# Performance work log

Hardware: AMD Instinct MI355X
Metric: run time of the kernel (lower is better)

## Reference

```python
import jax, jax.numpy as jnp
import numpy as np

N = 20000; P = 3; L_LP = 10; L_NS = 20; D = 128; OUT = 2; E = 640000; V_LP = 5000; V_NS = 10000


def _gru(x, lengths, W_ih, W_hh, b_ih, b_hh):
    # x: [B, T, Din]; returns last valid hidden state per sequence (pack_padded semantics)
    T = x.shape[1]
    xp = jnp.einsum('btd,gd->btg', x, W_ih) + b_ih  # [B, T, 3H]
    h0 = jnp.zeros((x.shape[0], W_hh.shape[1]), x.dtype)

    def step(h, inp):
        xpt, t = inp
        hp = h @ W_hh.T + b_hh
        xr, xz, xn = jnp.split(xpt, 3, axis=-1)
        hr, hz, hn = jnp.split(hp, 3, axis=-1)
        r = jax.nn.sigmoid(xr + hr)
        z = jax.nn.sigmoid(xz + hz)
        nn_ = jnp.tanh(xn + r * hn)
        h_new = (1.0 - z) * nn_ + z * h
        h = jnp.where((t < lengths)[:, None], h_new, h)
        return h, None

    hT, _ = jax.lax.scan(step, h0, (jnp.swapaxes(xp, 0, 1), jnp.arange(T)))
    return hT


def _gcn(x, src, dst, w, W, b, n):
    # PyG GCNConv: add self-loops (weight 1), symmetric normalization by in-degree
    loops = jnp.arange(n)
    s = jnp.concatenate([src, loops])
    d = jnp.concatenate([dst, loops])
    ww = jnp.concatenate([w, jnp.ones((n,), w.dtype)])
    deg = jax.ops.segment_sum(ww, d, num_segments=n)
    dinv = jnp.where(deg > 0, 1.0 / jnp.sqrt(deg), 0.0)
    norm = dinv[s] * ww * dinv[d]
    xw = x @ W.T
    return jax.ops.segment_sum(norm[:, None] * xw[s], d, num_segments=n) + b


def _lnorm(x, g, b):
    m = jnp.mean(x, axis=-1, keepdims=True)
    v = jnp.var(x, axis=-1, keepdims=True)
    return (x - m) / jnp.sqrt(v + 1e-5) * g + b


def _forward(x_ref, x_def, x_pdt, edge_weight, lp_emb, ns_emb, lp_Wih, lp_Whh, lp_bih, lp_bhh, ns_Wih, ns_Whh, ns_bih, ns_bhh, lp_fc_W, lp_fc_b, all_fc_W, all_fc_b, conv1_W, conv1_b, conv2_W, conv2_b, conv3_W, conv3_b, ln1_g, ln1_b, ln2_g, ln2_b, mp1_W, mp1_b, mp2_W, mp2_b, idx_lp, x_lp_length, idx_ns, x_ns_length, edge_index):
    n = idx_ns.shape[0]
    # long-path GRU encodings, one GRU run per path slot (vmapped over P)
    xl = lp_emb[idx_lp]  # [N, P, L_LP, D]
    gru_lp = lambda seq, lens: _gru(seq, lens, lp_Wih, lp_Whh, lp_bih, lp_bhh)
    h_lp = jax.vmap(gru_lp, in_axes=(1, 1))(xl, x_lp_length)  # [P, N, D]
    # torch.cat(h_list).view(N, D*P): row-major reshape of [P, N, D]
    x_lp = h_lp.reshape(n, P * D) @ lp_fc_W.T + lp_fc_b
    # natural-sequence GRU encoding
    x_ns = _gru(ns_emb[idx_ns], x_ns_length, ns_Wih, ns_Whh, ns_bih, ns_bhh)  # [N, D]
    # torch.cat(dim=0).view(N, 5D): faithful row-major reshape of [5N, D]
    x = jnp.concatenate([x_pdt, x_ref, x_def, x_lp, x_ns], axis=0).reshape(n, 5 * D)
    x = x @ all_fc_W.T + all_fc_b
    src, dst = edge_index[0], edge_index[1]
    convs = [(conv1_W, conv1_b), (conv2_W, conv2_b), (conv3_W, conv3_b)]
    lns = [(ln1_g, ln1_b), (ln2_g, ln2_b)]
    emb = x
    for i in range(3):
        x = _gcn(x, src, dst, edge_weight, convs[i][0], convs[i][1], n)
        emb = x
        x = jax.nn.relu(x)
        # dropout p=0.25 omitted (eval mode)
        if i < 2:
            x = _lnorm(x, lns[i][0], lns[i][1])
    x = x @ mp1_W.T + mp1_b
    x = x @ mp2_W.T + mp2_b
    return emb, jax.nn.log_softmax(x, axis=1)


def setup_inputs() -> dict:
    ks = jax.random.split(jax.random.key(0), 40)
    f32 = jnp.float32
    nrm = lambda k, sh, s: jax.random.normal(k, sh, f32) * s
    inp = {}
    inp['idx_lp'] = jax.random.randint(ks[0], (N, P, L_LP), 0, V_LP)
    inp['x_lp_length'] = jax.random.randint(ks[1], (N, P), 1, L_LP + 1)
    inp['idx_ns'] = jax.random.randint(ks[2], (N, L_NS), 0, V_NS)
    inp['x_ns_length'] = jax.random.randint(ks[3], (N,), 1, L_NS + 1)
    inp['x_ref'] = nrm(ks[4], (N, D), 1.0)
    inp['x_def'] = nrm(ks[5], (N, D), 1.0)
    inp['x_pdt'] = nrm(ks[6], (N, D), 1.0)
    inp['edge_index'] = jax.random.randint(ks[7], (2, E), 0, N)
    inp['edge_weight'] = jax.random.uniform(ks[8], (E,), f32)
    inp['lp_emb'] = nrm(ks[9], (V_LP, D), 0.5)
    inp['ns_emb'] = nrm(ks[10], (V_NS, D), 0.5)
    s = 0.08
    inp['lp_Wih'] = nrm(ks[11], (3 * D, D), s)
    inp['lp_Whh'] = nrm(ks[12], (3 * D, D), s)
    inp['lp_bih'] = nrm(ks[13], (3 * D,), s)
    inp['lp_bhh'] = nrm(ks[14], (3 * D,), s)
    inp['ns_Wih'] = nrm(ks[15], (3 * D, D), s)
    inp['ns_Whh'] = nrm(ks[16], (3 * D, D), s)
    inp['ns_bih'] = nrm(ks[17], (3 * D,), s)
    inp['ns_bhh'] = nrm(ks[18], (3 * D,), s)
    inp['lp_fc_W'] = nrm(ks[19], (D, P * D), 0.05)
    inp['lp_fc_b'] = nrm(ks[20], (D,), 0.05)
    inp['all_fc_W'] = nrm(ks[21], (D, 5 * D), 0.05)
    inp['all_fc_b'] = nrm(ks[22], (D,), 0.05)
    inp['conv1_W'] = nrm(ks[23], (D, D), 0.08)
    inp['conv1_b'] = nrm(ks[24], (D,), 0.05)
    inp['conv2_W'] = nrm(ks[25], (D, D), 0.08)
    inp['conv2_b'] = nrm(ks[26], (D,), 0.05)
    inp['conv3_W'] = nrm(ks[27], (D, D), 0.08)
    inp['conv3_b'] = nrm(ks[28], (D,), 0.05)
    inp['ln1_g'] = jnp.ones((D,), f32)
    inp['ln1_b'] = jnp.zeros((D,), f32)
    inp['ln2_g'] = jnp.ones((D,), f32)
    inp['ln2_b'] = jnp.zeros((D,), f32)
    inp['mp1_W'] = nrm(ks[29], (D, D), 0.08)
    inp['mp1_b'] = nrm(ks[30], (D,), 0.05)
    inp['mp2_W'] = nrm(ks[31], (OUT, D), 0.08)
    inp['mp2_b'] = nrm(ks[32], (OUT,), 0.05)
    return inp


def reference(idx_lp, x_lp_length, idx_ns, x_ns_length, x_ref, x_def, x_pdt, edge_index, edge_weight, lp_emb, ns_emb, lp_Wih, lp_Whh, lp_bih, lp_bhh, ns_Wih, ns_Whh, ns_bih, ns_bhh, lp_fc_W, lp_fc_b, all_fc_W, all_fc_b, conv1_W, conv1_b, conv2_W, conv2_b, conv3_W, conv3_b, ln1_g, ln1_b, ln2_g, ln2_b, mp1_W, mp1_b, mp2_W, mp2_b):
    return _forward(x_ref, x_def, x_pdt, edge_weight, lp_emb, ns_emb, lp_Wih, lp_Whh, lp_bih, lp_bhh, ns_Wih, ns_Whh, ns_bih, ns_bhh, lp_fc_W, lp_fc_b, all_fc_W, all_fc_b, conv1_W, conv1_b, conv2_W, conv2_b, conv3_W, conv3_b, ln1_g, ln1_b, ln2_g, ln2_b, mp1_W, mp1_b, mp2_W, mp2_b, idx_lp, x_lp_length, idx_ns, x_ns_length, edge_index)
```

## Files before the change

kernel.cpp:

```cpp
#include <hip/hip_runtime.h>
#include <math.h>

typedef unsigned short u16;
typedef short bf16x4 __attribute__((ext_vector_type(4)));
typedef short bf16x8 __attribute__((ext_vector_type(8)));
typedef float f32x16 __attribute__((ext_vector_type(16)));

#define NN 20000
#define PP 3
#define TLP 10
#define TNS 20
#define DD 128
#define EE 640000

__device__ __forceinline__ float bf2f(u16 u) {
  union { unsigned u; float f; } v; v.u = ((unsigned)u) << 16; return v.f;
}
__device__ __forceinline__ u16 f2bf(float f) {
  union { float f; unsigned u; } v; v.f = f;
  unsigned r = v.u + 0x7fffu + ((v.u >> 16) & 1u);
  return (u16)(r >> 16);
}
__device__ __forceinline__ short f2bf_hw(float f) {
  __bf16 b = (__bf16)f;
  return (short)__builtin_bit_cast(unsigned short, b);
}
__device__ __forceinline__ float loadf(const void* p, size_t i, int isf) {
  return isf ? ((const float*)p)[i] : bf2f(((const u16*)p)[i]);
}
__device__ __forceinline__ float fex2(float x) { return __builtin_amdgcn_exp2f(x); }
__device__ __forceinline__ float frcp(float x) { return __builtin_amdgcn_rcpf(x); }
__device__ __forceinline__ unsigned cvtpk(float lo, float hi) {
  unsigned r; asm("v_cvt_pk_bf16_f32 %0, %1, %2" : "=v"(r) : "v"(lo), "v"(hi));
  return r;
}

__global__ void k_detect(const void* probe, int* flag, int* bins) {
  __shared__ int any;
  if (threadIdx.x == 0) any = 0;
  __syncthreads();
  if (threadIdx.x < 128) bins[threadIdx.x] = 0;
  const u16* p = (const u16*)probe;
  int bad = 0;
  for (int i = threadIdx.x; i < 4096; i += 256) {
    int e = (p[2 * i] >> 7) & 0xFF;
    if (e >= 0x9F) bad = 1;
  }
  if (bad) atomicOr(&any, 1);
  __syncthreads();
  if (threadIdx.x == 0) flag[0] = any;
}

struct CvtJobs {
  const void* src[16];
  int off[16];
  int n[16];
};

struct CvtJobsB {
  const void* src[12];
  int off[12];
  int n[12];
  int thr[12];
  float scA[12];
  float scB[12];
};

__global__ void k_cvtb(CvtJobsB j, CvtJobs jf, u16* __restrict__ dst,
                       float* __restrict__ fdst, int* __restrict__ counts,
                       const int* flag) {
  const int isf = flag[0];
  if (blockIdx.x >= 12 * 64 + 16) {
    int i = (blockIdx.x - (12 * 64 + 16)) * 256 + threadIdx.x;
    if (i < NN) counts[i] = 0;
    return;
  }
  if (blockIdx.x >= 12 * 64) {
    const int job = blockIdx.x - 12 * 64;
    const void* s = jf.src[job];
    float* d = fdst + jf.off[job];
    const int n = jf.n[job];
    for (int i = threadIdx.x; i < n; i += 256) d[i] = loadf(s, i, isf);
    return;
  }
  const int job = blockIdx.x >> 6;
  if (job < 2 && !isf) return;
  const int chunk = blockIdx.x & 63;
  const void* s = j.src[job];
  u16* d = dst + j.off[job];
  const int n = j.n[job];
  const int thr = j.thr[job];
  const float sA = j.scA[job], sB = j.scB[job];
  for (int i = chunk * 256 + threadIdx.x; i < n; i += 64 * 256)
    d[i] = f2bf(loadf(s, i, isf) * (i < thr ? sA : sB));
}

__global__ void k_lenboth(const int* __restrict__ lensLP,
                          const int* __restrict__ lensNS,
                          int* __restrict__ bins,
                          const int* __restrict__ e_dst,
                          int* __restrict__ counts) {
  const int nLen = (PP * NN + 255) / 256;
  if ((int)blockIdx.x >= nLen) {
    int e = ((int)blockIdx.x - nLen) * 256 + threadIdx.x;
    if (e < EE) atomicAdd(&counts[e_dst[e]], 1);
    return;
  }
  int sg = blockIdx.x * 256 + threadIdx.x;
  int lane = threadIdx.x & 63;
  int binL = 0, binN = 0;
  if (sg < PP * NN) binL = lensLP[(sg % NN) * PP + sg / NN];
  if (sg < NN) binN = lensNS[sg];
  for (int b = 1; b <= TLP; ++b) {
    unsigned long long m = __ballot(binL == b);
    if (m) {
      int leader = (int)(__ffsll((long long)m) - 1);
      if (lane == leader) atomicAdd(&bins[b], (int)__popcll(m));
    }
  }
  for (int b = 1; b <= TNS; ++b) {
    unsigned long long m = __ballot(binN == b);
    if (m) {
      int leader = (int)(__ffsll((long long)m) - 1);
      if (lane == leader) atomicAdd(&bins[64 + b], (int)__popcll(m));
    }
  }
}

__global__ void k_binscan2(int* __restrict__ bins,
                           const float* __restrict__ w_mp2,
                           const float* __restrict__ b_mp1_,
                           const float* __restrict__ b_mp2_,
                           const void* __restrict__ mp1raw,
                           float* __restrict__ Wc, const int* flag) {
  if (blockIdx.x == 0) {
    if (threadIdx.x == 0) {
      int acc = 0;
      for (int k = 0; k < 32; ++k) { bins[32 + k] = acc; acc += bins[k]; }
    }
    if (threadIdx.x == 1) {
      int acc = 0;
      for (int k = 0; k < 32; ++k) { bins[96 + k] = acc; acc += bins[64 + k]; }
    }
    return;
  }
  const int isf = flag[0];
  const int t = threadIdx.x;
  const int o = t >> 7, k = t & 127;
  float acc = 0.f;
  for (int d2 = 0; d2 < 128; ++d2)
    acc += w_mp2[o * 128 + d2] * loadf(mp1raw, (size_t)d2 * 128 + k, isf);
  Wc[t] = acc;
  if (t < 2) {
    float bacc = b_mp2_[t];
    for (int d2 = 0; d2 < 128; ++d2) bacc += w_mp2[t * 128 + d2] * b_mp1_[d2];
    Wc[256 + t] = bacc;
  }
}

__global__ void k_lenfillboth(const int* __restrict__ lensLP,
                              const int* __restrict__ lensNS,
                              int* __restrict__ bins,
                              int* __restrict__ permLP,
                              int* __restrict__ permNS) {
  int sg = blockIdx.x * 256 + threadIdx.x;
  int lane = threadIdx.x & 63;
  int binL = 0, binN = 0;
  if (sg < PP * NN) binL = lensLP[(sg % NN) * PP + sg / NN];
  if (sg < NN) binN = lensNS[sg];
  for (int b = 1; b <= TLP; ++b) {
    unsigned long long m = __ballot(binL == b);
    if (m) {
      int leader = (int)(__ffsll((long long)m) - 1);
      int base = 0;
      if (lane == leader) base = atomicAdd(&bins[32 + b], (int)__popcll(m));
      base = __shfl(base, leader);
      if (binL == b) {
        int rank = (int)__popcll(m & ((1ull << lane) - 1ull));
        permLP[base + rank] = sg;
      }
    }
  }
  for (int b = 1; b <= TNS; ++b) {
    unsigned long long m = __ballot(binN == b);
    if (m) {
      int leader = (int)(__ffsll((long long)m) - 1);
      int base = 0;
      if (lane == leader) base = atomicAdd(&bins[96 + b], (int)__popcll(m));
      base = __shfl(base, leader);
      if (binN == b) {
        int rank = (int)__popcll(m & ((1ull << lane) - 1ull));
        permNS[base + rank] = sg;
      }
    }
  }
}

__global__ __launch_bounds__(512, 2) void k_gru5(
    const int* __restrict__ permLP, const int* __restrict__ permNS, int nbNS,
    const u16* __restrict__ embLPc, const u16* __restrict__ embNSc,
    const u16* __restrict__ embLPr, const u16* __restrict__ embNSr,
    const int* __restrict__ idxLP, const int* __restrict__ idxNS,
    const int* __restrict__ lenLP, const int* __restrict__ lenNS,
    const u16* __restrict__ WihLP, const u16* __restrict__ WhhLP,
    const u16* __restrict__ WihNS, const u16* __restrict__ WhhNS,
    const float* __restrict__ bihLP, const float* __restrict__ bhhLP,
    const float* __restrict__ bihNS, const float* __restrict__ bhhNS,
    u16* __restrict__ HoutLP, u16* __restrict__ HoutNS, int nbLP,
    const int* __restrict__ counts, int* __restrict__ startA,
    int* __restrict__ cursorE, const int* __restrict__ flag) {
  __shared__ u16 xp[2][3][128][36];
  __shared__ u16 Hbf2[2][32][132];
  __shared__ int ivs[TNS][32];
  __shared__ int rowv[32], outv[32], lenv_s[32];
  __shared__ int Tbs;

  const int tid = threadIdx.x;
  if (blockIdx.x == 0) {
    int* part = (int*)ivs;
    const int C = (NN + 255) / 256;
    if (tid < 256) {
      int base = tid * C;
      int s = 0;
      for (int k = 0; k < C; ++k) {
        int i2 = base + k;
        s += (i2 < NN) ? counts[i2] : 0;
      }
      part[tid] = s;
    }
    __syncthreads();
    if (tid == 0) {
      int acc = 0;
      for (int k = 0; k < 256; ++k) { int v = part[k]; part[k] = acc; acc += v; }
    }
    __syncthreads();
    if (tid < 256) {
      int run = part[tid];
      int base = tid * C;
      for (int k = 0; k < C; ++k) {
        int i2 = base + k;
        if (i2 < NN) {
          int c = counts[i2];
          startA[i2] = run;
          cursorE[i2] = run;
          run += c;
        }
      }
      if (tid == 255) startA[NN] = run;
    }
    return;
  }
  const int bid = blockIdx.x - 1;
  const int isf = flag[0];
  const int isNS = bid < nbNS;
  const int chunk = isNS ? (nbNS - 1 - bid) : (nbLP - 1 - (bid - nbNS));
  const int* perm = isNS ? (permNS + chunk * 32) : (permLP + chunk * 32);
  const u16* embbf = isNS ? (isf ? embNSc : embNSr) : (isf ? embLPc : embLPr);
  const int* idx = isNS ? idxNS : idxLP;
  const int* lens = isNS ? lenNS : lenLP;
  const u16* Wih = isNS ? WihNS : WihLP;
  const u16* Whh = isNS ? WhhNS : WhhLP;
  const float* bih = isNS ? bihNS : bihLP;
  const float* bhh = isNS ? bhhNS : bhhLP;
  u16* Hout = isNS ? HoutNS : HoutLP;
  const int T = isNS ? TNS : TLP;

  const int w = tid >> 6, lane = tid & 63;
  const int l31 = lane & 31, lh = lane >> 5;
  const int role = w >> 2;
  const int j = w & 3;
  const int d = 32 * j + l31;

  if (tid < 32) {
    int sg = perm[tid];
    int row = isNS ? sg : ((sg % NN) * PP + sg / NN);
    rowv[tid] = row;
    outv[tid] = sg;
    lenv_s[tid] = lens[row];
  }
  __syncthreads();
  if (tid == 0) {
    int m = 1;
    for (int k = 0; k < 32; ++k) m = max(m, lenv_s[k]);
    Tbs = m;
  }
  __syncthreads();
  const int Tb = Tbs;

  for (int z = tid; z < Tb * 32; z += 512) {
    int s = z & 31, t = z >> 5;
    ivs[t][s] = idx[(size_t)rowv[s] * T + t];
  }
  for (int z = tid; z < 2112; z += 512) ((unsigned*)Hbf2[0])[z] = 0u;

  bf16x8 wf[24];
  {
    const u16* Ws = role ? Whh : Wih;
#pragma unroll
    for (int g = 0; g < 3; ++g)
#pragma unroll
      for (int kb = 0; kb < 8; ++kb)
        wf[g * 8 + kb] =
            *(const bf16x8*)(Ws + (size_t)(128 * g + d) * 128 + kb * 16 + lh * 8);
  }
  const float SA = -1.44269504088896f;
  const float SN = -2.88539008177793f;
  float ib0, ib1, ib2;
  if (!role) {
    ib0 = SA * (bih[d] + bhh[d]);
    ib1 = SA * (bih[128 + d] + bhh[128 + d]);
    ib2 = SN * bih[256 + d];
  } else {
    ib0 = 0.f;
    ib1 = 0.f;
    ib2 = SN * bhh[256 + d];
  }

  __syncthreads();
  int lenr[16];
#pragma unroll
  for (int rg = 0; rg < 16; ++rg)
    lenr[rg] = lenv_s[(rg & 3) + 8 * (rg >> 2) + 4 * lh];

  float h[16];
#pragma unroll
  for (int rg = 0; rg < 16; ++rg) h[rg] = 0.f;

  for (int i = 0; i <= Tb; ++i) {
    if (!role) {
      if (i < Tb) {
        bf16x8 Xf[8];
        const u16* erow = embbf + (size_t)ivs[i][l31] * 128 + lh * 8;
#pragma unroll
        for (int kb = 0; kb < 8; ++kb) Xf[kb] = *(const bf16x8*)(erow + kb * 16);
        f32x16 a0 = (f32x16)(ib0), a1 = (f32x16)(ib1), a2 = (f32x16)(ib2);
#pragma unroll
        for (int kb = 0; kb < 8; ++kb) {
          a0 = __builtin_amdgcn_mfma_f32_32x32x16_bf16(Xf[kb], wf[kb], a0, 0, 0, 0);
          a1 = __builtin_amdgcn_mfma_f32_32x32x16_bf16(Xf[kb], wf[8 + kb], a1, 0, 0, 0);
          a2 = __builtin_amdgcn_mfma_f32_32x32x16_bf16(Xf[kb], wf[16 + kb], a2, 0, 0, 0);
        }
        const int sl = i & 1;
#pragma unroll
        for (int rq = 0; rq < 4; ++rq) {
          int mo = 8 * rq + 4 * lh;
          bf16x4 p0, p1, p2;
#pragma unroll
          for (int q = 0; q < 4; ++q) {
            p0[q] = f2bf_hw(a0[4 * rq + q]);
            p1[q] = f2bf_hw(a1[4 * rq + q]);
            p2[q] = f2bf_hw(a2[4 * rq + q]);
          }
          *(bf16x4*)(&xp[sl][0][d][mo]) = p0;
          *(bf16x4*)(&xp[sl][1][d][mo]) = p1;
          *(bf16x4*)(&xp[sl][2][d][mo]) = p2;
        }
      }
    } else {
      if (i >= 1) {
        const int rs = (i - 1) & 1, wsl = i & 1;
        bf16x8 Hf[8];
#pragma unroll
        for (int kb = 0; kb < 8; ++kb) {
          bf16x4 lo = *(const bf16x4*)(&Hbf2[rs][l31][16 * kb + 8 * lh]);
          bf16x4 hi = *(const bf16x4*)(&Hbf2[rs][l31][16 * kb + 8 * lh + 4]);
          Hf[kb] = __builtin_shufflevector(lo, hi, 0, 1, 2, 3, 4, 5, 6, 7);
        }
        f32x16 a0 = (f32x16)(ib0), a1 = (f32x16)(ib1), a2 = (f32x16)(ib2);
#pragma unroll
        for (int kb = 0; kb < 8; ++kb) {
          a0 = __builtin_amdgcn_mfma_f32_32x32x16_bf16(Hf[kb], wf[kb], a0, 0, 0, 0);
          a1 = __builtin_amdgcn_mfma_f32_32x32x16_bf16(Hf[kb], wf[8 + kb], a1, 0, 0, 0);
          a2 = __builtin_amdgcn_mfma_f32_32x32x16_bf16(Hf[kb], wf[16 + kb], a2, 0, 0, 0);
        }
        const int t = i - 1;
#pragma unroll
        for (int rq = 0; rq < 4; ++rq) {
          int mo = 8 * rq + 4 * lh;
          bf16x4 x0 = *(const bf16x4*)(&xp[rs][0][d][mo]);
          bf16x4 x1 = *(const bf16x4*)(&xp[rs][1][d][mo]);
          bf16x4 x2 = *(const bf16x4*)(&xp[rs][2][d][mo]);
          float hq[4];
#pragma unroll
          for (int q = 0; q < 4; ++q) {
            int rg = 4 * rq + q;
            float r = frcp(1.f + fex2(a0[rg] + bf2f((u16)x0[q])));
            float z = frcp(1.f + fex2(a1[rg] + bf2f((u16)x1[q])));
            float s = fmaf(r, a2[rg], bf2f((u16)x2[q]));
            float nn_ = fmaf(2.f, frcp(1.f + fex2(s)), -1.f);
            float hnew = fmaf(z, h[rg] - nn_, nn_);
            h[rg] = (t < lenr[rg]) ? hnew : h[rg];
            hq[q] = h[rg];
          }
          unsigned pa = cvtpk(hq[0], hq[1]);
          unsigned pb = cvtpk(hq[2], hq[3]);
          Hbf2[wsl][mo + 0][d] = (u16)pa;
          Hbf2[wsl][mo + 1][d] = (u16)(pa >> 16);
          Hbf2[wsl][mo + 2][d] = (u16)pb;
          Hbf2[wsl][mo + 3][d] = (u16)(pb >> 16);
        }
      }
    }
    __syncthreads();
  }

  if (role) {
#pragma unroll
    for (int rg = 0; rg < 16; ++rg) {
      int m = (rg & 3) + 8 * (rg >> 2) + 4 * lh;
      Hout[(size_t)outv[m] * 128 + d] = f2bf(h[rg]);
    }
  }
}

__global__ __launch_bounds__(128) void k_gemm_mfma(
    const void* __restrict__ A0, const void* __restrict__ A1,
    const void* __restrict__ A2, const u16* __restrict__ A3,
    const u16* __restrict__ A4, int mode, int K,
    const u16* __restrict__ W, const float* __restrict__ bias,
    void* __restrict__ Cout, int out_bf, int M, const int* __restrict__ flag,
    const int* __restrict__ esrc, const int* __restrict__ edst,
    const void* __restrict__ ew, int* __restrict__ cursor,
    int2* __restrict__ csr, const int* __restrict__ startT,
    float* __restrict__ dinvOut, int tailN, int tailMode, int gemmBlocks) {
  const int isf = flag[0];
  const int tid = threadIdx.x;
  if ((int)blockIdx.x >= gemmBlocks) {
    int i = ((int)blockIdx.x - gemmBlocks) * 128 + tid;
    if (i < tailN) {
      if (tailMode == 1) {
        int s = esrc[i];
        float wv = loadf(ew, i, isf);
        int p = atomicAdd(&cursor[edst[i]], 1);
        csr[p] = make_int2(s, __float_as_int(wv));
      } else {
        int a = startT[i], b = startT[i + 1];
        float sum = 1.f;
        for (int k = a; k < b; ++k) sum += __int_as_float(csr[k].y);
        dinvOut[i] = 1.f / sqrtf(sum);
      }
    }
    return;
  }
  const int w = tid >> 6, lane = tid & 63;
  const int l31 = lane & 31, lh = lane >> 5;
  const int w23 = w;
  const int mbase = blockIdx.x * 32;
  const int row = mbase + l31;
  const int rowc = row < M ? row : M - 1;

  f32x16 acc0 = (f32x16)(0.f), acc1 = (f32x16)(0.f);
  const int nk = K >> 4;
  for (int kb = 0; kb < nk; ++kb) {
    bf16x8 a;
    if (mode == 0) {
      a = *(const bf16x8*)((const u16*)A0 + (size_t)rowc * K + kb * 16 + lh * 8);
    } else {
      int r5 = 5 * rowc + (kb >> 3);
      int slot = r5 / NN;
      int inner = r5 - slot * NN;
      int koff = (kb & 7) * 16 + lh * 8;
      if (slot < 3) {
        const void* p = (slot == 0) ? A0 : (slot == 1) ? A1 : A2;
        if (isf) {
          const float* fp = (const float*)p + (size_t)inner * 128 + koff;
          float4 v0 = *(const float4*)fp;
          float4 v1 = *(const float4*)(fp + 4);
          a[0] = (short)f2bf(v0.x); a[1] = (short)f2bf(v0.y);
          a[2] = (short)f2bf(v0.z); a[3] = (short)f2bf(v0.w);
          a[4] = (short)f2bf(v1.x); a[5] = (short)f2bf(v1.y);
          a[6] = (short)f2bf(v1.z); a[7] = (short)f2bf(v1.w);
        } else {
          a = *(const bf16x8*)((const u16*)p + (size_t)inner * 128 + koff);
        }
      } else {
        const u16* p = (slot == 3) ? A3 : A4;
        a = *(const bf16x8*)(p + (size_t)inner * 128 + koff);
      }
    }
    const u16* wp = W + (size_t)(64 * w23 + l31) * K + kb * 16 + lh * 8;
    bf16x8 b0 = *(const bf16x8*)wp;
    bf16x8 b1 = *(const bf16x8*)(wp + (size_t)32 * K);
    acc0 = __builtin_amdgcn_mfma_f32_32x32x16_bf16(a, b0, acc0, 0, 0, 0);
    acc1 = __builtin_amdgcn_mfma_f32_32x32x16_bf16(a, b1, acc1, 0, 0, 0);
  }
  const int col0 = 64 * w23 + l31;
  const float bv0 = bias ? bias[col0] : 0.f;
  const float bv1 = bias ? bias[col0 + 32] : 0.f;
#pragma unroll
  for (int rg = 0; rg < 16; ++rg) {
    int m = (rg & 3) + 8 * (rg >> 2) + 4 * lh;
    int grow = mbase + m;
    if (grow < M) {
      float v0 = acc0[rg] + bv0, v1 = acc1[rg] + bv1;
      if (out_bf) {
        ((u16*)Cout)[(size_t)grow * 128 + col0] = f2bf(v0);
        ((u16*)Cout)[(size_t)grow * 128 + col0 + 32] = f2bf(v1);
      } else {
        ((float*)Cout)[(size_t)grow * 128 + col0] = v0;
        ((float*)Cout)[(size_t)grow * 128 + col0 + 32] = v1;
      }
    }
  }
}

__global__ __launch_bounds__(256) void k_gcn_gather(
    const int* __restrict__ start, const int2* __restrict__ csr,
    const float* __restrict__ dinv, const u16* __restrict__ xwbf,
    const float* __restrict__ bias, const float* __restrict__ g,
    const float* __restrict__ b, u16* __restrict__ out_bf,
    void* __restrict__ dout, const float* __restrict__ Wc,
    const int* __restrict__ flag, int mode) {
  int v = blockIdx.x * 4 + (threadIdx.x >> 6);
  int lane = threadIdx.x & 63;
  if (v >= NN) return;
  const int c0 = 2 * lane;
  float acc0 = 0.f, acc1 = 0.f;
  int i = start[v];
  const int i1 = start[v + 1];
  for (; i + 4 <= i1; i += 4) {
    int2 e0 = csr[i], e1 = csr[i + 1], e2 = csr[i + 2], e3 = csr[i + 3];
    unsigned p0 = *(const unsigned*)(xwbf + (size_t)e0.x * 128 + c0);
    unsigned p1 = *(const unsigned*)(xwbf + (size_t)e1.x * 128 + c0);
    unsigned p2 = *(const unsigned*)(xwbf + (size_t)e2.x * 128 + c0);
    unsigned p3 = *(const unsigned*)(xwbf + (size_t)e3.x * 128 + c0);
    float f0 = __int_as_float(e0.y) * dinv[e0.x];
    float f1 = __int_as_float(e1.y) * dinv[e1.x];
    float f2 = __int_as_float(e2.y) * dinv[e2.x];
    float f3 = __int_as_float(e3.y) * dinv[e3.x];
    acc0 += f0 * bf2f((u16)(p0 & 0xffff)) + f1 * bf2f((u16)(p1 & 0xffff)) +
            f2 * bf2f((u16)(p2 & 0xffff)) + f3 * bf2f((u16)(p3 & 0xffff));
    acc1 += f0 * bf2f((u16)(p0 >> 16)) + f1 * bf2f((u16)(p1 >> 16)) +
            f2 * bf2f((u16)(p2 >> 16)) + f3 * bf2f((u16)(p3 >> 16));
  }
  if (i + 2 <= i1) {
    int2 e0 = csr[i], e1 = csr[i + 1];
    unsigned p0 = *(const unsigned*)(xwbf + (size_t)e0.x * 128 + c0);
    unsigned p1 = *(const unsigned*)(xwbf + (size_t)e1.x * 128 + c0);
    float f0 = __int_as_float(e0.y) * dinv[e0.x];
    float f1 = __int_as_float(e1.y) * dinv[e1.x];
    acc0 += f0 * bf2f((u16)(p0 & 0xffff)) + f1 * bf2f((u16)(p1 & 0xffff));
    acc1 += f0 * bf2f((u16)(p0 >> 16)) + f1 * bf2f((u16)(p1 >> 16));
    i += 2;
  }
  if (i < i1) {
    int2 e = csr[i];
    float c = __int_as_float(e.y) * dinv[e.x];
    unsigned pv = *(const unsigned*)(xwbf + (size_t)e.x * 128 + c0);
    acc0 += c * bf2f((u16)(pv & 0xffff));
    acc1 += c * bf2f((u16)(pv >> 16));
  }
  float dv = dinv[v];
  unsigned sv = *(const unsigned*)(xwbf + (size_t)v * 128 + c0);
  float y0 = bias[c0] + dv * (dv * bf2f((u16)(sv & 0xffff)) + acc0);
  float y1 = bias[c0 + 1] + dv * (dv * bf2f((u16)(sv >> 16)) + acc1);
  if (mode == 1) {
    if (flag[0]) {
      *(float2*)((float*)dout + (size_t)v * 128 + c0) = make_float2(y0, y1);
    } else {
      unsigned pk = (unsigned)f2bf(y0) | ((unsigned)f2bf(y1) << 16);
      *(unsigned*)((u16*)dout + (size_t)v * 128 + c0) = pk;
    }
    float x0 = fmaxf(y0, 0.f), x1 = fmaxf(y1, 0.f);
    float p0 = x0 * Wc[c0] + x1 * Wc[c0 + 1];
    float p1 = x0 * Wc[128 + c0] + x1 * Wc[128 + c0 + 1];
#pragma unroll
    for (int off = 32; off; off >>= 1) {
      p0 += __shfl_xor(p0, off);
      p1 += __shfl_xor(p1, off);
    }
    if (lane == 0) {
      float v0 = p0 + Wc[256], v1 = p1 + Wc[257];
      float m = fmaxf(v0, v1);
      float ls = m + logf(__expf(v0 - m) + __expf(v1 - m));
      size_t base = (size_t)NN * 128 + (size_t)v * 2;
      if (flag[0]) {
        ((float*)dout)[base + 0] = v0 - ls;
        ((float*)dout)[base + 1] = v1 - ls;
      } else {
        unsigned pk = (unsigned)f2bf(v0 - ls) | ((unsigned)f2bf(v1 - ls) << 16);
        *(unsigned*)((u16*)dout + base) = pk;
      }
    }
  } else {
    float x0 = fmaxf(y0, 0.f), x1 = fmaxf(y1, 0.f);
    float s_ = x0 + x1;
#pragma unroll
    for (int off = 32; off; off >>= 1) s_ += __shfl_xor(s_, off);
    float mean = s_ * (1.f / 128.f);
    float e0 = x0 - mean, e1 = x1 - mean;
    float vv = e0 * e0 + e1 * e1;
#pragma unroll
    for (int off = 32; off; off >>= 1) vv += __shfl_xor(vv, off);
    float inv = 1.f / sqrtf(vv * (1.f / 128.f) + 1e-5f);
    unsigned pk = (unsigned)f2bf(e0 * inv * g[c0] + b[c0]) |
                  ((unsigned)f2bf(e1 * inv * g[c0 + 1] + b[c0 + 1]) << 16);
    *(unsigned*)(out_bf + (size_t)v * 128 + c0) = pk;
  }
}

extern "C" void kernel_launch(void* const* d_in, const int* in_sizes, int n_in,
                              void* d_out, int out_size, void* d_ws, size_t ws_size,
                              hipStream_t stream) {
  const int* idx_lp = (const int*)d_in[0];
  const int* len_lp = (const int*)d_in[1];
  const int* idx_ns = (const int*)d_in[2];
  const int* len_ns = (const int*)d_in[3];
  const void* x_ref = d_in[4];
  const void* x_def = d_in[5];
  const void* x_pdt = d_in[6];
  const int* eidx   = (const int*)d_in[7];
  const void* ew    = d_in[8];
  const void* lp_emb = d_in[9];
  const void* ns_emb = d_in[10];

  char* cur = (char*)d_ws;
  auto alloc = [&](size_t bytes, size_t align) -> void* {
    size_t a = ((size_t)cur + align - 1) & ~(align - 1);
    cur = (char*)(a + bytes);
    return (void*)a;
  };
  int* flag     = (int*)alloc(64, 64);
  float* smallW = (float*)alloc(3104 * 4, 16);
  float* f_Wc   = (float*)alloc(260 * 4, 16);
  float* f_dinv = (float*)alloc(NN * 4, 16);
  int* counts   = (int*)alloc(NN * 4, 16);
  int* startA   = (int*)alloc((NN + 1) * 4, 16);
  int* cursorE  = (int*)alloc(NN * 4, 16);
  int* bins     = (int*)alloc(128 * 4, 16);
  int* perm_lp  = (int*)alloc(PP * NN * 4, 16);
  int* perm_ns  = (int*)alloc(NN * 4, 16);
  int2* csr2    = (int2*)alloc((size_t)EE * 8, 16);
  u16* ub       = (u16*)alloc((size_t)20233216 * 2, 16);
  u16* embbf_lp = ub;
  u16* embbf_ns = ub + 640000;
  u16* wg_lpih  = ub + 1920000;
  u16* wg_lphh  = ub + 1969152;
  u16* wg_nsih  = ub + 2018304;
  u16* wg_nshh  = ub + 2067456;
  u16* wg_lpfc  = ub + 2116608;
  u16* wg_allfc = ub + 2165760;
  u16* wg_c1    = ub + 2247680;
  u16* wg_c2    = ub + 2264064;
  u16* wg_c3    = ub + 2280448;
  u16* hbf_lp   = ub + 2313216;
  u16* hbf_ns   = ub + 9993216;
  u16* lp_bf    = ub + 12553216;
  u16* xcur_bf  = ub + 15113216;
  u16* xw_bf    = ub + 17673216;

  static const int fn[16] = {384, 384, 384, 384, 128, 128, 128, 128,
                             128, 128, 128, 128, 128, 128, 256, 2};
  static const int fsrc[16] = {13, 14, 17, 18, 20, 22, 24, 26,
                               28, 29, 30, 31, 32, 34, 35, 36};
  CvtJobs jf;
  int foff[16];
  {
    int off = 0;
    for (int j = 0; j < 16; ++j) {
      jf.src[j] = d_in[fsrc[j]];
      jf.off[j] = off;
      jf.n[j] = fn[j];
      foff[j] = off;
      off += fn[j];
    }
  }
  float* b_lpbih = smallW + foff[0];
  float* b_lpbhh = smallW + foff[1];
  float* b_nsbih = smallW + foff[2];
  float* b_nsbhh = smallW + foff[3];
  float* b_lpfc  = smallW + foff[4];
  float* b_allfc = smallW + foff[5];
  float* b_conv[3] = {smallW + foff[6], smallW + foff[7], smallW + foff[8]};
  float* g_ln[2] = {smallW + foff[9], smallW + foff[11]};
  float* b_ln[2] = {smallW + foff[10], smallW + foff[12]};
  float* b_mp1   = smallW + foff[13];
  float* w_mp2   = smallW + foff[14];
  float* b_mp2   = smallW + foff[15];

  static const int bn[12] = {640000, 1280000, 49152, 49152, 49152, 49152,
                             49152, 81920, 16384, 16384, 16384, 0};
  static const int bsrc[12] = {9, 10, 11, 12, 15, 16, 19, 21, 23, 25, 27, 33};
  static const int boff[12] = {0, 640000, 1920000, 1969152, 2018304, 2067456,
                               2116608, 2165760, 2247680, 2264064, 2280448,
                               2296832};
  CvtJobsB jb;
  for (int j = 0; j < 12; ++j) {
    jb.src[j] = d_in[bsrc[j]];
    jb.off[j] = boff[j];
    jb.n[j] = bn[j];
    const bool gw = (j >= 2 && j <= 5);
    jb.thr[j] = gw ? 32768 : 0;
    jb.scA[j] = gw ? -1.44269504088896f : 1.f;
    jb.scB[j] = gw ? -2.88539008177793f : 1.f;
  }

  const int* e_src = eidx;
  const int* e_dst = eidx + EE;

  k_detect<<<1, 256, 0, stream>>>(lp_emb, flag, bins);

  const int initBlocks = (NN + 255) / 256;
  k_cvtb<<<12 * 64 + 16 + initBlocks, 256, 0, stream>>>(jb, jf, ub, smallW,
                                                        counts, flag);

  const int lenBlocks = (PP * NN + 255) / 256;
  const int histBlocks = (EE + 255) / 256;
  k_lenboth<<<lenBlocks + histBlocks, 256, 0, stream>>>(len_lp, len_ns, bins,
                                                        e_dst, counts);
  k_binscan2<<<2, 256, 0, stream>>>(bins, w_mp2, b_mp1, b_mp2, d_in[33],
                                    f_Wc, flag);
  k_lenfillboth<<<lenBlocks, 256, 0, stream>>>(len_lp, len_ns, bins,
                                               perm_lp, perm_ns);

  const int nbLP = PP * NN / 32, nbNS = NN / 32;
  k_gru5<<<1 + nbLP + nbNS, 512, 0, stream>>>(
      perm_lp, perm_ns, nbNS, embbf_lp, embbf_ns,
      (const u16*)lp_emb, (const u16*)ns_emb,
      idx_lp, idx_ns, len_lp, len_ns,
      wg_lpih, wg_lphh, wg_nsih, wg_nshh, b_lpbih, b_lpbhh, b_nsbih, b_nsbhh,
      hbf_lp, hbf_ns, nbLP, counts, startA, cursorE, flag);

  const int gg = (NN + 31) / 32;
  const int fillBlocks = (EE + 127) / 128;
  const int degBlocks = (NN + 127) / 128;
  k_gemm_mfma<<<gg + fillBlocks, 128, 0, stream>>>(
      hbf_lp, nullptr, nullptr, nullptr, nullptr, 0, 384, wg_lpfc, b_lpfc,
      lp_bf, 1, NN, flag, e_src, e_dst, ew, cursorE, csr2, nullptr, nullptr,
      EE, 1, gg);
  k_gemm_mfma<<<gg + degBlocks, 128, 0, stream>>>(
      x_pdt, x_ref, x_def, lp_bf, hbf_ns, 1, 640, wg_allfc, b_allfc,
      xcur_bf, 1, NN, flag, nullptr, nullptr, nullptr, nullptr, csr2, startA,
      f_dinv, NN, 2, gg);

  const u16* wgc[3] = {wg_c1, wg_c2, wg_c3};
  for (int l = 0; l < 3; ++l) {
    k_gemm_mfma<<<gg, 128, 0, stream>>>(
        xcur_bf, nullptr, nullptr, nullptr, nullptr, 0, DD, wgc[l], nullptr,
        xw_bf, 1, NN, flag, nullptr, nullptr, nullptr, nullptr, nullptr,
        nullptr, nullptr, 0, 0, gg);
    if (l < 2) {
      k_gcn_gather<<<NN / 4, 256, 0, stream>>>(startA, csr2, f_dinv, xw_bf,
                                               b_conv[l], g_ln[l], b_ln[l],
                                               xcur_bf, nullptr, nullptr,
                                               flag, 0);
    } else {
      k_gcn_gather<<<NN / 4, 256, 0, stream>>>(startA, csr2, f_dinv, xw_bf,
                                               b_conv[l], nullptr, nullptr,
                                               nullptr, d_out, f_Wc,
                                               flag, 1);
    }
  }
}
```

Baseline: 845.2 us.

## Merge conversion, length histogram, edge histogram and Wc precompute into one launch

Folds the bf16/fp32 conversion, the length-bin and edge-degree histograms, and the mp2·mp1 weight folding into a single kernel. The counts zeroing moves into the detect launch. The bin prefix scan is dropped: the fill kernel now builds per-bin offsets inline by summing bin counts. This cuts two kernel launches and their serialization, at the cost of each fill thread re-reading the bin counts and the fused kernel reading raw inputs instead of converted buffers.

```diff
diff --git a/kernel.cpp b/kernel.cpp
--- a/kernel.cpp
+++ b/kernel.cpp
@@ -35,7 +35,13 @@
   return r;
 }
 
-__global__ void k_detect(const void* probe, int* flag, int* bins) {
+__global__ void k_detect(const void* probe, int* flag, int* bins,
+                         int* __restrict__ counts) {
+  if (blockIdx.x > 0) {
+    int i = (blockIdx.x - 1) * 256 + threadIdx.x;
+    if (i < NN) counts[i] = 0;
+    return;
+  }
   __shared__ int any;
   if (threadIdx.x == 0) any = 0;
   __syncthreads();
@@ -66,95 +72,85 @@
   float scB[12];
 };
 
-__global__ void k_cvtb(CvtJobsB j, CvtJobs jf, u16* __restrict__ dst,
-                       float* __restrict__ fdst, int* __restrict__ counts,
-                       const int* flag) {
+__global__ void k_megacvt(CvtJobsB j, CvtJobs jf, u16* __restrict__ dst,
+                          float* __restrict__ fdst,
+                          const int* __restrict__ lensLP,
+                          const int* __restrict__ lensNS,
+                          int* __restrict__ bins,
+                          const int* __restrict__ e_dst,
+                          int* __restrict__ counts,
+                          const void* __restrict__ w2raw,
+                          const void* __restrict__ b1raw,
+                          const void* __restrict__ b2raw,
+                          const void* __restrict__ mp1raw,
+                          float* __restrict__ Wc, const int* flag) {
   const int isf = flag[0];
-  if (blockIdx.x >= 12 * 64 + 16) {
-    int i = (blockIdx.x - (12 * 64 + 16)) * 256 + threadIdx.x;
-    if (i < NN) counts[i] = 0;
+  const int B_CVT = 12 * 64;
+  const int B_F = B_CVT + 16;
+  const int LEN_B = (PP * NN + 255) / 256;
+  const int B_LEN = B_F + LEN_B;
+  const int HIST_B = (EE + 255) / 256;
+  const int B_HIST = B_LEN + HIST_B;
+  const int bx = (int)blockIdx.x;
+  const int tid = threadIdx.x;
+  if (bx < B_CVT) {
+    const int job = bx >> 6;
+    if (job < 2 && !isf) return;
+    const int chunk = bx & 63;
+    const void* s = j.src[job];
+    u16* d = dst + j.off[job];
+    const int n = j.n[job];
+    const int thr = j.thr[job];
+    const float sA = j.scA[job], sB = j.scB[job];
+    for (int i = chunk * 256 + tid; i < n; i += 64 * 256)
+      d[i] = f2bf(loadf(s, i, isf) * (i < thr ? sA : sB));
     return;
   }
-  if (blockIdx.x >= 12 * 64) {
-    const int job = blockIdx.x - 12 * 64;
+  if (bx < B_F) {
+    const int job = bx - B_CVT;
     const void* s = jf.src[job];
     float* d = fdst + jf.off[job];
     const int n = jf.n[job];
-    for (int i = threadIdx.x; i < n; i += 256) d[i] = loadf(s, i, isf);
+    for (int i = tid; i < n; i += 256) d[i] = loadf(s, i, isf);
     return;
   }
-  const int job = blockIdx.x >> 6;
-  if (job < 2 && !isf) return;
-  const int chunk = blockIdx.x & 63;
-  const void* s = j.src[job];
-  u16* d = dst + j.off[job];
-  const int n = j.n[job];
-  const int thr = j.thr[job];
-  const float sA = j.scA[job], sB = j.scB[job];
-  for (int i = chunk * 256 + threadIdx.x; i < n; i += 64 * 256)
-    d[i] = f2bf(loadf(s, i, isf) * (i < thr ? sA : sB));
-}
-
-__global__ void k_lenboth(const int* __restrict__ lensLP,
-                          const int* __restrict__ lensNS,
-                          int* __restrict__ bins,
-                          const int* __restrict__ e_dst,
-                          int* __restrict__ counts) {
-  const int nLen = (PP * NN + 255) / 256;
-  if ((int)blockIdx.x >= nLen) {
-    int e = ((int)blockIdx.x - nLen) * 256 + threadIdx.x;
+  if (bx < B_LEN) {
+    int sg = (bx - B_F) * 256 + tid;
+    int lane = tid & 63;
+    int binL = 0, binN = 0;
+    if (sg < PP * NN) binL = lensLP[(sg % NN) * PP + sg / NN];
+    if (sg < NN) binN = lensNS[sg];
+    for (int b = 1; b <= TLP; ++b) {
+      unsigned long long m = __ballot(binL == b);
+      if (m) {
+        int leader = (int)(__ffsll((long long)m) - 1);
+        if (lane == leader) atomicAdd(&bins[b], (int)__popcll(m));
+      }
+    }
+    for (int b = 1; b <= TNS; ++b) {
+      unsigned long long m = __ballot(binN == b);
+      if (m) {
+        int leader = (int)(__ffsll((long long)m) - 1);
+        if (lane == leader) atomicAdd(&bins[64 + b], (int)__popcll(m));
+      }
+    }
+    return;
+  }
+  if (bx < B_HIST) {
+    int e = (bx - B_LEN) * 256 + tid;
     if (e < EE) atomicAdd(&counts[e_dst[e]], 1);
     return;
   }
-  int sg = blockIdx.x * 256 + threadIdx.x;
-  int lane = threadIdx.x & 63;
-  int binL = 0, binN = 0;
-  if (sg < PP * NN) binL = lensLP[(sg % NN) * PP + sg / NN];
-  if (sg < NN) binN = lensNS[sg];
-  for (int b = 1; b <= TLP; ++b) {
-    unsigned long long m = __ballot(binL == b);
-    if (m) {
-      int leader = (int)(__ffsll((long long)m) - 1);
-      if (lane == leader) atomicAdd(&bins[b], (int)__popcll(m));
-    }
-  }
-  for (int b = 1; b <= TNS; ++b) {
-    unsigned long long m = __ballot(binN == b);
-    if (m) {
-      int leader = (int)(__ffsll((long long)m) - 1);
-      if (lane == leader) atomicAdd(&bins[64 + b], (int)__popcll(m));
-    }
-  }
-}
-
-__global__ void k_binscan2(int* __restrict__ bins,
-                           const float* __restrict__ w_mp2,
-                           const float* __restrict__ b_mp1_,
-                           const float* __restrict__ b_mp2_,
-                           const void* __restrict__ mp1raw,
-                           float* __restrict__ Wc, const int* flag) {
-  if (blockIdx.x == 0) {
-    if (threadIdx.x == 0) {
-      int acc = 0;
-      for (int k = 0; k < 32; ++k) { bins[32 + k] = acc; acc += bins[k]; }
-    }
-    if (threadIdx.x == 1) {
-      int acc = 0;
-      for (int k = 0; k < 32; ++k) { bins[96 + k] = acc; acc += bins[64 + k]; }
-    }
-    return;
-  }
-  const int isf = flag[0];
-  const int t = threadIdx.x;
-  const int o = t >> 7, k = t & 127;
+  const int o = tid >> 7, k = tid & 127;
   float acc = 0.f;
   for (int d2 = 0; d2 < 128; ++d2)
-    acc += w_mp2[o * 128 + d2] * loadf(mp1raw, (size_t)d2 * 128 + k, isf);
-  Wc[t] = acc;
-  if (t < 2) {
-    float bacc = b_mp2_[t];
-    for (int d2 = 0; d2 < 128; ++d2) bacc += w_mp2[t * 128 + d2] * b_mp1_[d2];
-    Wc[256 + t] = bacc;
+    acc += loadf(w2raw, o * 128 + d2, isf) * loadf(mp1raw, (size_t)d2 * 128 + k, isf);
+  Wc[tid] = acc;
+  if (tid < 2) {
+    float bacc = loadf(b2raw, tid, isf);
+    for (int d2 = 0; d2 < 128; ++d2)
+      bacc += loadf(w2raw, tid * 128 + d2, isf) * loadf(b1raw, d2, isf);
+    Wc[256 + tid] = bacc;
   }
 }
 
@@ -168,6 +164,7 @@
   int binL = 0, binN = 0;
   if (sg < PP * NN) binL = lensLP[(sg % NN) * PP + sg / NN];
   if (sg < NN) binN = lensNS[sg];
+  int baseL = 0;
   for (int b = 1; b <= TLP; ++b) {
     unsigned long long m = __ballot(binL == b);
     if (m) {
@@ -177,10 +174,12 @@
       base = __shfl(base, leader);
       if (binL == b) {
         int rank = (int)__popcll(m & ((1ull << lane) - 1ull));
-        permLP[base + rank] = sg;
-      }
-    }
-  }
+        permLP[baseL + base + rank] = sg;
+      }
+    }
+    baseL += bins[b];
+  }
+  int baseN = 0;
   for (int b = 1; b <= TNS; ++b) {
     unsigned long long m = __ballot(binN == b);
     if (m) {
@@ -190,9 +189,10 @@
       base = __shfl(base, leader);
       if (binN == b) {
         int rank = (int)__popcll(m & ((1ull << lane) - 1ull));
-        permNS[base + rank] = sg;
-      }
-    }
+        permNS[baseN + base + rank] = sg;
+      }
+    }
+    baseN += bins[64 + b];
   }
 }
 
@@ -674,9 +674,6 @@
   float* b_conv[3] = {smallW + foff[6], smallW + foff[7], smallW + foff[8]};
   float* g_ln[2] = {smallW + foff[9], smallW + foff[11]};
   float* b_ln[2] = {smallW + foff[10], smallW + foff[12]};
-  float* b_mp1   = smallW + foff[13];
-  float* w_mp2   = smallW + foff[14];
-  float* b_mp2   = smallW + foff[15];
 
   static const int bn[12] = {640000, 1280000, 49152, 49152, 49152, 49152,
                              49152, 81920, 16384, 16384, 16384, 0};
@@ -698,18 +695,15 @@
   const int* e_src = eidx;
   const int* e_dst = eidx + EE;
 
-  k_detect<<<1, 256, 0, stream>>>(lp_emb, flag, bins);
-
   const int initBlocks = (NN + 255) / 256;
-  k_cvtb<<<12 * 64 + 16 + initBlocks, 256, 0, stream>>>(jb, jf, ub, smallW,
-                                                        counts, flag);
+  k_detect<<<1 + initBlocks, 256, 0, stream>>>(lp_emb, flag, bins, counts);
 
   const int lenBlocks = (PP * NN + 255) / 256;
   const int histBlocks = (EE + 255) / 256;
-  k_lenboth<<<lenBlocks + histBlocks, 256, 0, stream>>>(len_lp, len_ns, bins,
-                                                        e_dst, counts);
-  k_binscan2<<<2, 256, 0, stream>>>(bins, w_mp2, b_mp1, b_mp2, d_in[33],
-                                    f_Wc, flag);
+  k_megacvt<<<12 * 64 + 16 + lenBlocks + histBlocks + 1, 256, 0, stream>>>(
+      jb, jf, ub, smallW, len_lp, len_ns, bins, e_dst, counts,
+      d_in[35], d_in[34], d_in[36], d_in[33], f_Wc, flag);
+
   k_lenfillboth<<<lenBlocks, 256, 0, stream>>>(len_lp, len_ns, bins,
                                                perm_lp, perm_ns);
 
```

Result: faster. 823.0 us (-2.6%).
